# Kernel optimization log

Hardware: AMD Instinct MI355X
Metric: run time of the kernel (lower is better)

Reference implementation:

```python
import jax, jax.numpy as jnp
import numpy as np

EPS = 1e-6
NUM_HEADS = 12


def ln_cf(x, w, b):
    # channels_first LayerNorm over channel dim (ConvNeXt style)
    u = jnp.mean(x, axis=1, keepdims=True)
    s = jnp.mean((x - u) ** 2, axis=1, keepdims=True)
    xn = (x - u) / jnp.sqrt(s + EPS)
    shp = (1, -1) + (1,) * (x.ndim - 2)
    return xn * w.reshape(shp) + b.reshape(shp)


def conv2s2(x, w):
    # Conv3d kernel=2 stride=2 (no bias): exact non-overlapping patch contraction
    b, c, H, W, D = x.shape
    xp = x.reshape(b, c, H // 2, 2, W // 2, 2, D // 2, 2)
    return jnp.einsum('bchkwpdq,ockpq->bohwd', xp, w)


def convt2s2(x, w):
    # ConvTranspose3d kernel=2 stride=2 (torch weight layout [in, out, 2,2,2])
    b, i, H, W, D = x.shape
    o = w.shape[1]
    y = jnp.einsum('bihwd,iokpq->bohkwpdq', x, w)
    return y.reshape(b, o, 2 * H, 2 * W, 2 * D)


def stem(x, w1, g1, b1, w2, g2, b2):
    h = conv2s2(x, w1)
    h = jax.nn.gelu(ln_cf(h, g1, b1), approximate=False)
    h = conv2s2(h, w2)
    return ln_cf(h, g2, b2)


def debed(x, tw1, g, b, tw2, tb2):
    h = convt2s2(x, tw1)
    h = jax.nn.gelu(ln_cf(h, g, b), approximate=False)
    return convt2s2(h, tw2) + tb2.reshape(1, -1, 1, 1, 1)


def rope(x):
    # rotary embedding over full token dim c (pairs (i, i+c/2)), positions 0..L-1
    b, l, c = x.shape
    inv = 1.0 / (10000.0 ** (jnp.arange(0, c, 2, dtype=jnp.float32) / c))
    t = jnp.arange(l, dtype=jnp.float32)
    f = jnp.outer(t, inv)                      # [l, c/2]
    emb = jnp.concatenate([f, f], axis=-1)     # [l, c]
    cos, sin = jnp.cos(emb)[None], jnp.sin(emb)[None]
    rot = jnp.concatenate([-x[..., c // 2:], x[..., :c // 2]], axis=-1)
    return x * cos + rot * sin


def _forward(x, skip, q_w1, q_g1, q_b1, q_w2, q_g2, q_b2,
             k_w1, k_g1, k_b1, k_w2, k_g2, k_b2,
             v_w1, v_g1, v_b1, v_w2, v_g2, v_b2,
             o_tw1, o_g, o_b, o_tw2, o_tb2,
             ns_w, ns_b, nx_w, nx_b, no_w, no_b):
    res = skip
    skip = ln_cf(skip, ns_w, ns_b)
    x = ln_cf(x, nx_w, nx_b)
    q = stem(skip, q_w1, q_g1, q_b1, q_w2, q_g2, q_b2)
    k = stem(x, k_w1, k_g1, k_b1, k_w2, k_g2, k_b2)
    v = stem(x, v_w1, v_g1, v_b1, v_w2, v_g2, v_b2)
    b, c, Hq, Wq, Dq = q.shape
    _, _, Hk, Wk, Dk = k.shape
    q = q.reshape(b, c, -1).transpose(0, 2, 1)   # [b, Lq, c]
    k = k.reshape(b, c, -1).transpose(0, 2, 1)   # [b, Lk, c]
    v = v.reshape(b, c, -1).transpose(0, 2, 1)
    q = rope(q)
    k = rope(k)
    hd = c // NUM_HEADS
    qh = q.reshape(b, -1, NUM_HEADS, hd).transpose(0, 2, 1, 3)  # [b, nh, Lq, hd]
    kh = k.reshape(b, -1, NUM_HEADS, hd).transpose(0, 2, 1, 3)
    vh = v.reshape(b, -1, NUM_HEADS, hd).transpose(0, 2, 1, 3)
    scale = 1.0 / jnp.sqrt(jnp.float32(hd))
    attn = jax.nn.softmax(jnp.einsum('bhqc,bhkc->bhqk', qh, kh) * scale, axis=-1)
    proj = jnp.einsum('bhqk,bhkc->bhqc', attn, vh)              # [b, nh, Lq, hd]
    # rearrange 'b nh l c -> b (c nh) h w d'
    proj = proj.transpose(0, 3, 1, 2).reshape(b, c, Hq, Wq, Dq)
    proj = ln_cf(proj, no_w, no_b)
    out = debed(proj, o_tw1, o_g, o_b, o_tw2, o_tb2)
    return out + res


def setup_inputs() -> dict:
    key = jax.random.key(0)
    ks = iter(jax.random.split(key, 40))
    def nrm(shape, scale):
        return jax.random.normal(next(ks), shape, jnp.float32) * scale
    E, E4, XF, SF = 768, 192, 6, 6
    inp = {
        'x': nrm((2, XF, 48, 48, 48), 1.0),
        'skip': nrm((2, SF, 48, 48, 48), 1.0),
    }
    for p, ic in [('q', SF), ('k', XF), ('v', XF)]:
        inp[p + '_w1'] = nrm((E4, ic, 2, 2, 2), (ic * 8) ** -0.5)
        inp[p + '_g1'] = jnp.ones(E4, jnp.float32)
        inp[p + '_b1'] = jnp.zeros(E4, jnp.float32)
        inp[p + '_w2'] = nrm((E, E4, 2, 2, 2), (E4 * 8) ** -0.5)
        inp[p + '_g2'] = jnp.ones(E, jnp.float32)
        inp[p + '_b2'] = jnp.zeros(E, jnp.float32)
    inp['o_tw1'] = nrm((E, E4, 2, 2, 2), E ** -0.5)
    inp['o_g'] = jnp.ones(E4, jnp.float32)
    inp['o_b'] = jnp.zeros(E4, jnp.float32)
    inp['o_tw2'] = nrm((E4, SF, 2, 2, 2), E4 ** -0.5)
    inp['o_tb2'] = jnp.zeros(SF, jnp.float32)
    inp['ns_w'] = jnp.ones(SF, jnp.float32)
    inp['ns_b'] = jnp.zeros(SF, jnp.float32)
    inp['nx_w'] = jnp.ones(XF, jnp.float32)
    inp['nx_b'] = jnp.zeros(XF, jnp.float32)
    inp['no_w'] = jnp.ones(E, jnp.float32)
    inp['no_b'] = jnp.zeros(E, jnp.float32)
    return inp


def reference(x, skip, q_w1, q_g1, q_b1, q_w2, q_g2, q_b2,
              k_w1, k_g1, k_b1, k_w2, k_g2, k_b2,
              v_w1, v_g1, v_b1, v_w2, v_g2, v_b2,
              o_tw1, o_g, o_b, o_tw2, o_tb2,
              ns_w, ns_b, nx_w, nx_b, no_w, no_b):
    return _forward(x, skip, q_w1, q_g1, q_b1, q_w2, q_g2, q_b2,
                    k_w1, k_g1, k_b1, k_w2, k_g2, k_b2,
                    v_w1, v_g1, v_b1, v_w2, v_g2, v_b2,
                    o_tw1, o_g, o_b, o_tw2, o_tb2,
                    ns_w, ns_b, nx_w, nx_b, no_w, no_b)
```

## Files before the change

kernel.cpp:

```cpp
#include <hip/hip_runtime.h>
#include <math.h>

#define BB_ 2
#define C0 6
#define S0 48
#define V0 (S0*S0*S0)
#define C1 192
#define S1 24
#define V1 (S1*S1*S1)
#define C2 768
#define S2 12
#define LL (S2*S2*S2)
#define NH 12
#define HD 64
#define KDIM (C1*8)
#define MDIM (BB_*LL)

typedef __attribute__((ext_vector_type(8))) short short8;
typedef __attribute__((ext_vector_type(4))) short short4v;
typedef __attribute__((ext_vector_type(4))) float float4v;

static __device__ __forceinline__ float gelu_exact(float x){
  return 0.5f*x*(1.0f+erff(x*0.70710678118654752440f));
}
static __device__ __forceinline__ unsigned short f2bf(float f){
  unsigned int u = __float_as_uint(f);
  unsigned int r = (u + 0x7fffu + ((u>>16)&1u)) >> 16;
  return (unsigned short)r;
}
static __device__ __forceinline__ unsigned int pk_bf16(float a, float b){
#if __has_builtin(__builtin_amdgcn_cvt_pk_bf16_f32)
  typedef __attribute__((ext_vector_type(2))) __bf16 bf2;
  bf2 r = __builtin_amdgcn_cvt_pk_bf16_f32(a,b);
  union { bf2 v; unsigned int u; } cv; cv.v = r;
  return cv.u;
#else
  return (unsigned int)f2bf(a) | ((unsigned int)f2bf(b)<<16);
#endif
}
static __device__ __forceinline__ float bf2f(unsigned short u){
  return __uint_as_float(((unsigned int)u)<<16);
}
static __device__ __forceinline__ float exp2v(float x){
#if __has_builtin(__builtin_amdgcn_exp2f)
  return __builtin_amdgcn_exp2f(x);
#else
  return exp2f(x);
#endif
}
static __device__ __forceinline__ void load_lds16(const void* g, void* l){
  __builtin_amdgcn_global_load_lds((const __attribute__((address_space(1))) unsigned int*)g,
      (__attribute__((address_space(3))) unsigned int*)l, 16, 0, 0);
}
static __device__ __forceinline__ float4v mfma32(short8 a, short8 b, float4v c){
  return __builtin_amdgcn_mfma_f32_16x16x32_bf16(a,b,c,0,0,0);
}
static __device__ __forceinline__ float4v mfma16(short4v a, short4v b, float4v c){
#if __has_builtin(__builtin_amdgcn_mfma_f32_16x16x16bf16_1k)
  return __builtin_amdgcn_mfma_f32_16x16x16bf16_1k(a,b,c,0,0,0);
#else
  asm volatile("v_mfma_f32_16x16x16_bf16 %0, %1, %2, %0" : "+v"(c) : "v"(a), "v"(b));
  return c;
#endif
}


__global__ __launch_bounds__(256) void prep_kernel(
    const float* __restrict__ skin, const float* __restrict__ xin,
    const float* __restrict__ nsw, const float* __restrict__ nsb,
    const float* __restrict__ nxw, const float* __restrict__ nxb,
    unsigned short* __restrict__ outS, unsigned short* __restrict__ outX,
    const float* __restrict__ qw2, const float* __restrict__ kw2, const float* __restrict__ vw2,
    const float* __restrict__ tw1, const float* __restrict__ tw2,
    const float* __restrict__ qw1, const float* __restrict__ kw1, const float* __restrict__ vw1,
    unsigned short* __restrict__ w2tq, unsigned short* __restrict__ w2tk,
    unsigned short* __restrict__ w2tv, unsigned short* __restrict__ Btd,
    unsigned short* __restrict__ Bt48,
    unsigned short* __restrict__ w1q, unsigned short* __restrict__ w1k,
    unsigned short* __restrict__ w1v){
  int bx = blockIdx.x;
  if (bx < 1728){
    int z = bx >= 864;
    const float* in = z ? xin : skin;
    const float* w  = z ? nxw : nsw;
    const float* bi = z ? nxb : nsb;
    unsigned short* out = z ? outX : outS;
    int idx = (bx - z*864)*256 + threadIdx.x;
    int b = idx / V0, vox = idx - b*V0;
    const float* p = in + (size_t)b*(C0*V0) + vox;
    float v[C0]; float s=0.f;
#pragma unroll
    for (int c=0;c<C0;c++){ v[c]=p[(size_t)c*V0]; s+=v[c]; }
    float u = s*(1.f/C0);
    float ss=0.f;
#pragma unroll
    for (int c=0;c<C0;c++){ float d=v[c]-u; ss+=d*d; }
    float inv = rsqrtf(ss*(1.f/C0)+1e-6f);
    unsigned short* o = out + (size_t)b*(C0*V0) + vox;
#pragma unroll
    for (int c=0;c<C0;c++) o[(size_t)c*V0] = f2bf((v[c]-u)*inv*w[c]+bi[c]);
    return;
  }
  bx -= 1728;
  if (bx < 13824){
    int z = bx/4608;
    int idx = (bx - z*4608)*256 + threadIdx.x;
    const float* w2 = (z==0)?qw2:((z==1)?kw2:vw2);
    unsigned short* o = (z==0)?w2tq:((z==1)?w2tk:w2tv);
    int oc = idx/KDIM; int k = idx-oc*KDIM; int p = k/C1; int ic = k-p*C1;
    size_t dst = ((size_t)(oc>>6)*48 + (k>>5))*2048 + (oc&63)*32 + (k&31);
    o[dst] = f2bf(w2[(size_t)oc*KDIM + ic*8 + p]);
  } else if (bx < 18432){
    int idx = (bx-13824)*256 + threadIdx.x;
    int n = idx/C2; int p = idx-n*C2;
    int i = ((p&63)*NH) + (p>>6);
    int kpq = n/C1, o2 = n-kpq*C1;
    size_t dst = ((size_t)(n>>6)*24 + (p>>5))*2048 + (n&63)*32 + (p&31);
    Btd[dst] = f2bf(tw1[(size_t)i*KDIM + o2*8 + kpq]);
  } else if (bx < 18480){
    int idx = (bx-18432)*256 + threadIdx.x;
    int n = idx/C1; int i = idx-n*C1;
    Bt48[idx] = (n<48) ? f2bf(tw2[(size_t)i*48 + n]) : (unsigned short)0;
  } else {
    int idx = (bx-18480)*256 + threadIdx.x;
    int z = idx / 9216; int r = idx - z*9216;
    const float* w1 = (z==0)?qw1:((z==1)?kw1:vw1);
    unsigned short* o = (z==0)?w1q:((z==1)?w1k:w1v);
    o[r] = f2bf(w1[r]);
  }
}

__global__ __launch_bounds__(256) void conv1_kernel(
    const unsigned short* __restrict__ lnSb, const unsigned short* __restrict__ lnXb,
    const unsigned short* __restrict__ w1bq, const unsigned short* __restrict__ w1bk,
    const unsigned short* __restrict__ w1bv,
    const float* __restrict__ qg1, const float* __restrict__ qb1,
    const float* __restrict__ kg1, const float* __restrict__ kb1,
    const float* __restrict__ vg1, const float* __restrict__ vb1,
    unsigned short* __restrict__ h1q, unsigned short* __restrict__ h1k,
    unsigned short* __restrict__ h1v){
  __shared__ __align__(16) unsigned short Ost[4][16*200];
  int z = blockIdx.z;
  const unsigned short* in = (z==0)? lnSb : lnXb;
  const unsigned short* Wb = (z==0)?w1bq:((z==1)?w1bk:w1bv);
  const float* g1 = (z==0)?qg1:((z==1)?kg1:vg1);
  const float* b1 = (z==0)?qb1:((z==1)?kb1:vb1);
  unsigned short* h1p = (z==0)?h1q:((z==1)?h1k:h1v);
  int t = threadIdx.x, w = t>>6, lane = t&63;
  int g = lane>>4, l16 = lane&15;
  int j = blockIdx.x*4 + w;
  int bxh = j/18, mt = j - bxh*18;
  int b = bxh/48; int rem = bxh - b*48; int y = rem>>1, xh = rem&1;
  int xo = mt/3, zo = mt - xo*3;
  int xv = xh*12 + xo*2 + (l16>>3);
  int zv = zo*8 + (l16&7);
  int x2 = 2*xv, z2 = 2*zv, y2 = 2*y;
  const unsigned short* base = in + (size_t)b*C0*V0;
  union { short8 v; unsigned int u[4]; } aA;
  {
    size_t rb = (size_t)g*V0;
    aA.u[0] = *(const unsigned int*)&base[rb + (y2+0)*(S0*S0) + (x2+0)*S0 + z2];
    aA.u[1] = *(const unsigned int*)&base[rb + (y2+0)*(S0*S0) + (x2+1)*S0 + z2];
    aA.u[2] = *(const unsigned int*)&base[rb + (y2+1)*(S0*S0) + (x2+0)*S0 + z2];
    aA.u[3] = *(const unsigned int*)&base[rb + (y2+1)*(S0*S0) + (x2+1)*S0 + z2];
  }
  union { short4v v; unsigned int u[2]; } aB;
  {
    size_t rb = (size_t)(4+(g>>1))*V0 + (y2+(g&1))*(S0*S0);
    aB.u[0] = *(const unsigned int*)&base[rb + (x2+0)*S0 + z2];
    aB.u[1] = *(const unsigned int*)&base[rb + (x2+1)*S0 + z2];
  }
  float4v acc[12];
#pragma unroll
  for (int ot=0; ot<12; ot++){
    short8  wA = *(const short8*)&Wb[(ot*16+l16)*48 + g*8];
    short4v wB = *(const short4v*)&Wb[(ot*16+l16)*48 + 32 + g*4];
    float4v a = {};
    a = mfma32(wA, aA.v, a);
    a = mfma16(wB, aB.v, a);
    acc[ot] = a;
  }
  float s1=0.f, s2=0.f;
#pragma unroll
  for (int ot=0;ot<12;ot++)
#pragma unroll
    for (int reg=0;reg<4;reg++){ float v=acc[ot][reg]; s1+=v; s2+=v*v; }
  s1 += __shfl_xor(s1,16); s1 += __shfl_xor(s1,32);
  s2 += __shfl_xor(s2,16); s2 += __shfl_xor(s2,32);
  float u = s1*(1.f/C1);
  float inv = rsqrtf(s2*(1.f/C1)-u*u+1e-6f);
  int tokbase = (y>>1)*(S2*S2) + (xh*6+xo)*S2 + zo*4;
  int m0_ = b*LL + tokbase;
  int panel = m0_>>7, row0 = m0_&127;
  int Y4 = (y&1)*4;
  int p8x = (l16>>3)*2 + (l16&1);
  int t2 = (l16&7)>>1;
  unsigned short* Lw = &Ost[w][(p8x*4+t2)*200];
#pragma unroll
  for (int ot=0; ot<12; ot++){
    int oc0 = ot*16 + g*4;
    float4 gg = *(const float4*)&g1[oc0];
    float4 bb = *(const float4*)&b1[oc0];
    float x0 = gelu_exact((acc[ot][0]-u)*inv*gg.x+bb.x);
    float x1 = gelu_exact((acc[ot][1]-u)*inv*gg.y+bb.y);
    float x2e= gelu_exact((acc[ot][2]-u)*inv*gg.z+bb.z);
    float x3 = gelu_exact((acc[ot][3]-u)*inv*gg.w+bb.w);
    uint2 pk; pk.x = pk_bf16(x0,x1); pk.y = pk_bf16(x2e,x3);
    *(uint2*)&Lw[oc0] = pk;
  }
  __syncthreads();
  unsigned short* pb2 = h1p + ((size_t)panel*48 + Y4*6)*4096 + row0*32;
#pragma unroll
  for (int it=0; it<6; it++){
    int flat = it*64 + lane;
    int c = flat>>4, s = flat&15;
    int pp = c/6, ocr = c - pp*6;
    uint4 d = *(const uint4*)&Ost[w][(pp*4 + (s>>2))*200 + ocr*32 + (s&3)*8];
    *(uint4*)&pb2[(size_t)c*4096 + (s>>2)*32 + (s&3)*8] = d;
  }
}

__global__ __launch_bounds__(256) void gemm_stem_kernel(
    const unsigned short* __restrict__ A0, const unsigned short* __restrict__ A1,
    const unsigned short* __restrict__ A2,
    const unsigned short* __restrict__ B0, const unsigned short* __restrict__ B1,
    const unsigned short* __restrict__ B2,
    unsigned short* __restrict__ Cq, unsigned short* __restrict__ Ck,
    unsigned short* __restrict__ Cv){
  int flat = blockIdx.x;
  int xcd = flat & 7, slot = flat >> 3;
  int tile = xcd*122 + slot;
  if (tile >= 972) return;
  int z = tile/324; int rr = tile - z*324;
  int mp = rr/12, np = rr - mp*12;
  const unsigned short* A = (z==0)?A0:((z==1)?A1:A2);
  const unsigned short* Bt = (z==0)?B0:((z==1)?B1:B2);
  unsigned short* Cp = (z==0)?Cq:((z==1)?Ck:Cv);
  __shared__ __align__(16) unsigned short Al[3][4096];
  __shared__ __align__(16) unsigned short Bl[3][2048];
  int t=threadIdx.x, w=t>>6, lane=t&63;
  int g=lane>>4, l16=lane&15;
  int wm=w>>1, wn=w&1;
  int loff = (lane>>2)*32 + (((lane&3) ^ ((lane>>3)&3))<<3);
  int crd  = (g ^ ((l16>>1)&3))*8;
  const unsigned short* gp[3];
  unsigned short* ld[3];
  int step[3];
#pragma unroll
  for (int cc=0;cc<3;cc++){
    int ch = w*3+cc;
    if (ch<8){
      gp[cc] = A + ((size_t)mp*48)*4096 + ch*512 + loff;
      step[cc] = 4096; ld[cc] = &Al[0][ch*512];
    } else {
      gp[cc] = Bt + ((size_t)np*48)*2048 + (ch-8)*512 + loff;
      step[cc] = 2048; ld[cc] = &Bl[0][(ch-8)*512];
    }
  }
  auto STAGE = [&](int buf){
#pragma unroll
    for (int cc=0;cc<3;cc++){
      load_lds16(gp[cc], ld[cc] + buf*step[cc]);
      gp[cc] += step[cc];
    }
  };
  float4v acc[4][2] = {};
  auto COMPUTE = [&](int buf){
    short8 af[4], bf[2];
#pragma unroll
    for (int mt=0;mt<4;mt++) af[mt] = *(const short8*)&Al[buf][(wm*64+mt*16+l16)*32 + crd];
#pragma unroll
    for (int nt=0;nt<2;nt++) bf[nt] = *(const short8*)&Bl[buf][(wn*32+nt*16+l16)*32 + crd];
#pragma unroll
    for (int mt=0;mt<4;mt++)
#pragma unroll
      for (int nt=0;nt<2;nt++)
        acc[mt][nt] = mfma32(af[mt], bf[nt], acc[mt][nt]);
  };
  const int NT = 48;
  STAGE(0); STAGE(1);
  asm volatile("s_waitcnt vmcnt(3)" ::: "memory");
  __builtin_amdgcn_s_barrier();
  __builtin_amdgcn_sched_barrier(0);
  int cur = 0;
  for (int tt=0; tt<NT-2; tt++){
    int nb = cur+2; if (nb>=3) nb-=3;
    STAGE(nb);
    COMPUTE(cur);
    asm volatile("s_waitcnt vmcnt(3)" ::: "memory");
    __builtin_amdgcn_s_barrier();
    __builtin_amdgcn_sched_barrier(0);
    cur++; if (cur>=3) cur-=3;
  }
  COMPUTE(cur);
  asm volatile("s_waitcnt vmcnt(0)" ::: "memory");
  __builtin_amdgcn_s_barrier();
  __builtin_amdgcn_sched_barrier(0);
  cur++; if (cur>=3) cur-=3;
  COMPUTE(cur);
  int m0 = mp*128, n0 = np*64;
#pragma unroll
  for (int mt=0;mt<4;mt++){
    int mb = m0 + wm*64 + mt*16 + g*4;
#pragma unroll
    for (int nt=0;nt<2;nt++){
      int col = n0 + wn*32 + nt*16 + l16;
#pragma unroll
      for (int reg=0;reg<4;reg++)
        Cp[(size_t)(mb+reg)*C2 + col] = f2bf(acc[mt][nt][reg]);
    }
  }
}

__global__ __launch_bounds__(256) void gemm_debed_kernel(const unsigned short* __restrict__ A,
    const unsigned short* __restrict__ Bt, unsigned short* __restrict__ C){
  int flat = blockIdx.x;
  int xcd = flat & 7, slot = flat >> 3;
  int tile = xcd*81 + slot;
  int mp = tile/24, np = tile - mp*24;
  __shared__ __align__(16) unsigned short Al[3][4096];
  __shared__ __align__(16) unsigned short Bl[3][2048];
  int t=threadIdx.x, w=t>>6, lane=t&63;
  int g=lane>>4, l16=lane&15;
  int wm=w>>1, wn=w&1;
  int loff = (lane>>2)*32 + (((lane&3) ^ ((lane>>3)&3))<<3);
  int crd  = (g ^ ((l16>>1)&3))*8;
  const unsigned short* gp[3];
  unsigned short* ld[3];
  int step[3];
#pragma unroll
  for (int cc=0;cc<3;cc++){
    int ch = w*3+cc;
    if (ch<8){
      gp[cc] = A + ((size_t)mp*24)*4096 + ch*512 + loff;
      step[cc] = 4096; ld[cc] = &Al[0][ch*512];
    } else {
      gp[cc] = Bt + ((size_t)np*24)*2048 + (ch-8)*512 + loff;
      step[cc] = 2048; ld[cc] = &Bl[0][(ch-8)*512];
    }
  }
  auto STAGE = [&](int buf){
#pragma unroll
    for (int cc=0;cc<3;cc++){
      load_lds16(gp[cc], ld[cc] + buf*step[cc]);
      gp[cc] += step[cc];
    }
  };
  float4v acc[4][2] = {};
  auto COMPUTE = [&](int buf){
    short8 af[4], bf[2];
#pragma unroll
    for (int mt=0;mt<4;mt++) af[mt] = *(const short8*)&Al[buf][(wm*64+mt*16+l16)*32 + crd];
#pragma unroll
    for (int nt=0;nt<2;nt++) bf[nt] = *(const short8*)&Bl[buf][(wn*32+nt*16+l16)*32 + crd];
#pragma unroll
    for (int mt=0;mt<4;mt++)
#pragma unroll
      for (int nt=0;nt<2;nt++)
        acc[mt][nt] = mfma32(af[mt], bf[nt], acc[mt][nt]);
  };
  const int NT = 24;
  STAGE(0); STAGE(1);
  asm volatile("s_waitcnt vmcnt(3)" ::: "memory");
  __builtin_amdgcn_s_barrier();
  __builtin_amdgcn_sched_barrier(0);
  int cur = 0;
  for (int tt=0; tt<NT-2; tt++){
    int nb = cur+2; if (nb>=3) nb-=3;
    STAGE(nb);
    COMPUTE(cur);
    asm volatile("s_waitcnt vmcnt(3)" ::: "memory");
    __builtin_amdgcn_s_barrier();
    __builtin_amdgcn_sched_barrier(0);
    cur++; if (cur>=3) cur-=3;
  }
  COMPUTE(cur);
  asm volatile("s_waitcnt vmcnt(0)" ::: "memory");
  __builtin_amdgcn_s_barrier();
  __builtin_amdgcn_sched_barrier(0);
  cur++; if (cur>=3) cur-=3;
  COMPUTE(cur);
  int m0 = mp*128, n0 = np*64;
#pragma unroll
  for (int nt=0;nt<2;nt++){
    int n = n0 + wn*32 + nt*16 + l16;
    int kpq = n / C1;
    int o = n - kpq*C1;
#pragma unroll
    for (int mt=0;mt<4;mt++){
      int mb = m0 + wm*64 + mt*16 + g*4;
#pragma unroll
      for (int reg=0;reg<4;reg++){
        int m = mb + reg;
        int b = m / LL; int tok = m - b*LL;
        int h = tok/(S2*S2), ww=(tok/S2)%S2, d=tok%S2;
        int v24 = (2*h+((kpq>>2)&1))*(S1*S1) + (2*ww+((kpq>>1)&1))*S1 + (2*d+(kpq&1));
        C[(size_t)(b*V1+v24)*C1 + o] = f2bf(acc[mt][nt][reg]);
      }
    }
  }
}

__global__ __launch_bounds__(256) void final_kernel(const unsigned short* __restrict__ dh,
    const unsigned short* __restrict__ Bt48, const float* __restrict__ og,
    const float* __restrict__ ob, const float* __restrict__ tb2s,
    const float* __restrict__ skipp, float* __restrict__ out){
  __shared__ __align__(16) unsigned short As[64*200];
  __shared__ __align__(16) unsigned short Bs[64*200];
  int t=threadIdx.x, w=t>>6, lane=t&63;
  int g=lane>>4, l16=lane&15;
  int m0 = blockIdx.x*64;
  for (int n8 = t; n8 < 1536; n8 += 256){
    int n64 = n8/24, kk = (n8 - n64*24)*8;
    uint4 d4 = *(const uint4*)&Bt48[n64*192 + kk];
    *(uint4*)&Bs[n64*200 + kk] = d4;
  }
  float g0=og[lane], g1v=og[lane+64], g2v=og[lane+128];
  float b0=ob[lane], b1v=ob[lane+64], b2v=ob[lane+128];
  for (int rr=0; rr<16; rr++){
    int rl = w*16 + rr;
    const unsigned short* row = dh + (size_t)(m0+rl)*C1;
    float v0=bf2f(row[lane]), v1=bf2f(row[lane+64]), v2=bf2f(row[lane+128]);
    float s1=v0+v1+v2, s2=v0*v0+v1*v1+v2*v2;
#pragma unroll
    for (int off=32;off>0;off>>=1){ s1+=__shfl_xor(s1,off); s2+=__shfl_xor(s2,off); }
    float u=s1*(1.f/C1), inv=rsqrtf(s2*(1.f/C1)-u*u+1e-6f);
    As[rl*200+lane]     = f2bf(gelu_exact((v0-u)*inv*g0+b0));
    As[rl*200+lane+64]  = f2bf(gelu_exact((v1-u)*inv*g1v+b1v));
    As[rl*200+lane+128] = f2bf(gelu_exact((v2-u)*inv*g2v+b2v));
  }
  __syncthreads();
  int wm=w>>1, wn=w&1;
  float4v acc[2][2] = {};
#pragma unroll
  for (int kb=0;kb<192;kb+=32){
    short8 af[2], bf[2];
#pragma unroll
    for (int mt=0;mt<2;mt++) af[mt] = *(const short8*)&As[(wm*32+mt*16+l16)*200 + kb + g*8];
#pragma unroll
    for (int nt=0;nt<2;nt++) bf[nt] = *(const short8*)&Bs[(wn*32+nt*16+l16)*200 + kb + g*8];
#pragma unroll
    for (int mt=0;mt<2;mt++)
#pragma unroll
      for (int nt=0;nt<2;nt++)
        acc[mt][nt] = mfma32(af[mt], bf[nt], acc[mt][nt]);
  }
#pragma unroll
  for (int nt=0;nt<2;nt++){
    int n = wn*32 + nt*16 + l16;
    if (n < 48){
      int c = n>>3, kpq = n&7;
      float bias = tb2s[c];
#pragma unroll
      for (int mt=0;mt<2;mt++){
        int mb = m0 + wm*32 + mt*16 + g*4;
#pragma unroll
        for (int reg=0;reg<4;reg++){
          int m = mb + reg;
          int b = m / V1; int v24 = m - b*V1;
          int y24 = v24/(S1*S1), x24=(v24/S1)%S1, z24=v24%S1;
          int vox = (2*y24+((kpq>>2)&1))*(S0*S0) + (2*x24+((kpq>>1)&1))*S0 + 2*z24+(kpq&1);
          size_t oi = (size_t)(b*C0+c)*V0 + vox;
          out[oi] = acc[mt][nt][reg] + bias + skipp[oi];
        }
      }
    }
  }
}

__global__ __launch_bounds__(256) void ln768_stem_kernel(
    unsigned short* __restrict__ qb, unsigned short* __restrict__ kb2,
    unsigned short* __restrict__ vb,
    const float* __restrict__ qg, const float* __restrict__ qbi,
    const float* __restrict__ kg, const float* __restrict__ kbi,
    const float* __restrict__ vg, const float* __restrict__ vbi, float qscale){
  int z = blockIdx.y;
  unsigned short* buf = (z==0)?qb:((z==1)?kb2:vb);
  const float* g  = (z==0)?qg:((z==1)?kg:vg);
  const float* bia= (z==0)?qbi:((z==1)?kbi:vbi);
  float scale = (z==0)? qscale : 1.0f;
  int tok = blockIdx.x*4 + (threadIdx.x>>6), lane = threadIdx.x&63;
  unsigned short* row = buf + (size_t)tok*C2;
  float v[12]; float s1=0.f,s2=0.f;
#pragma unroll
  for (int i=0;i<12;i++){ float t=bf2f(row[i*64+lane]); v[i]=t; s1+=t; s2+=t*t; }
#pragma unroll
  for (int off=32;off>0;off>>=1){ s1+=__shfl_xor(s1,off); s2+=__shfl_xor(s2,off); }
  float u=s1*(1.f/C2);
  float inv=rsqrtf(s2*(1.f/C2)-u*u+1e-6f);
  if (z==2){
#pragma unroll
    for (int i=0;i<12;i++){ int j=i*64+lane; row[j]=f2bf((v[i]-u)*inv*g[j]+bia[j]); }
  } else {
    int pos = tok % LL;
#pragma unroll
    for (int i=0;i<6;i++){
      int j=i*64+lane;
      float xn1=(v[i]-u)*inv*g[j]+bia[j];
      float xn2=(v[i+6]-u)*inv*g[j+384]+bia[j+384];
      float fr=(float)pos*__expf(-0.02398526139f*(float)j);
      float cs=cosf(fr), sn=sinf(fr);
      row[j]     = f2bf((xn1*cs - xn2*sn)*scale);
      row[j+384] = f2bf((xn2*cs + xn1*sn)*scale);
    }
  }
}

__global__ __launch_bounds__(256) void vtrans_kernel(const unsigned short* __restrict__ vbf,
    unsigned short* __restrict__ vT){
  __shared__ unsigned short T[64*72];
  int tok0 = blockIdx.x*64;
  int h = blockIdx.y, b = blockIdx.z;
  int t = threadIdx.x;
#pragma unroll
  for (int i=0;i<2;i++){
    int idx = t + i*256;
    int token = idx>>3, dc = idx&7;
    uint4 d4 = *(const uint4*)&vbf[(size_t)(b*LL+tok0+token)*C2 + h*64 + dc*8];
    const unsigned short* s = (const unsigned short*)&d4;
#pragma unroll
    for (int j2=0;j2<8;j2++) T[(dc*8+j2)*72 + token] = s[j2];
  }
  __syncthreads();
  int r = t>>2, seg = t&3;
  unsigned short* dst = vT + (size_t)((b*NH+h)*HD + r)*LL + tok0 + seg*16;
  uint4 o[2];
  unsigned short* os = (unsigned short*)o;
#pragma unroll
  for (int j2=0;j2<16;j2++) os[j2] = T[r*72 + seg*16 + j2];
  *(uint4*)dst = o[0];
  *(uint4*)(dst+8) = o[1];
}

__global__ __launch_bounds__(256) void attn_kernel(const unsigned short* __restrict__ q,
    const unsigned short* __restrict__ k, const unsigned short* __restrict__ vt,
    unsigned short* __restrict__ opart, float* __restrict__ lbuf){
  __shared__ __align__(16) unsigned char smem[32768];
  unsigned short* Ks = (unsigned short*)smem;
  unsigned short* Vs = Ks + 4096;
  int flat = blockIdx.x;
  int xcd = flat & 7, slot = flat >> 3;
  int tile = xcd*108 + slot;
  int h = tile / 72; int rem = tile - h*72;
  int zb = rem / 9, qt = rem - zb*9;
  int b = zb >> 2, split = zb & 3;
  int t=threadIdx.x, w=t>>6, lane=t&63;
  int g=lane>>4, l16=lane&15;
  short8 qA[3], qB[3];
#pragma unroll
  for (int j=0;j<3;j++){
    const unsigned short* qrow = q + (size_t)(b*LL + qt*192 + w*48 + j*16 + l16)*C2 + h*64;
    qA[j] = *(const short8*)(qrow + g*8);
    qB[j] = *(const short8*)(qrow + 32 + g*8);
  }
  const unsigned short* kbase = k + (size_t)(b*LL)*C2 + h*64;
  const unsigned short* vbase = vt + (size_t)((b*NH+h)*HD)*LL;
  int sub = lane>>3;
  int chs = (lane&7) ^ sub;
  int ktb = split*7, kte = (split==3)? 27 : (split*7+7);
  const unsigned short* gptr[4];
  unsigned short* ldst[4];
  int gstep[4];
#pragma unroll
  for (int cc=0;cc<4;cc++){
    int ii = w*4+cc;
    if (ii<8){
      int key = ktb*64 + ii*8 + sub;
      gptr[cc] = kbase + (size_t)key*C2 + chs*8;
      gstep[cc] = 64*C2;
      ldst[cc] = &Ks[ii*512];
    } else {
      int d = (ii-8)*8 + sub;
      gptr[cc] = vbase + (size_t)d*LL + ktb*64 + chs*8;
      gstep[cc] = 64;
      ldst[cc] = &Vs[(ii-8)*512];
    }
  }
  int sw = l16 & 7;
  const unsigned short* ksrow = &Ks[l16*64 + (g^sw)*8];
  int c2d = (((4+g)^sw) - (g^sw))*8;
  const unsigned short* vsrow = &Vs[l16*64 + (g&1)*4];
  int xk[4];
#pragma unroll
  for (int kc=0;kc<4;kc++) xk[kc] = (((kc*2 + (g>>1)) ^ sw))*8;
  short4v vones;
  vones[0]=vones[1]=vones[2]=vones[3]=(short)0x3F80;
  float4v O4[3][4] = {};
  float4v Ol[3] = {};
#pragma unroll
  for (int cc=0;cc<4;cc++){
    load_lds16(gptr[cc], ldst[cc]);
    gptr[cc] += gstep[cc];
  }
  __syncthreads();
  int cur = 0;
  for (int kt=ktb; kt<kte; kt++){
    if (kt+1 < kte){
      int so = (cur^1)*8192;
#pragma unroll
      for (int cc=0;cc<4;cc++){
        load_lds16(gptr[cc], ldst[cc]+so);
        gptr[cc] += gstep[cc];
      }
    }
    int co = cur*8192;
    const unsigned short* kr = ksrow + co;
    const unsigned short* vr = vsrow + co;
    float4v sc[3][4];
#pragma unroll
    for (int nt=0;nt<4;nt++){
      short8 k1 = *(const short8*)(kr + nt*1024);
      short8 k2 = *(const short8*)(kr + nt*1024 + c2d);
#pragma unroll
      for (int j=0;j<3;j++){
        float4v zz = {};
        zz = mfma32(k1, qA[j], zz);
        zz = mfma32(k2, qB[j], zz);
        sc[j][nt] = zz;
      }
    }
#pragma unroll
    for (int j=0;j<3;j++)
#pragma unroll
      for (int nt=0;nt<4;nt++)
#pragma unroll
        for (int reg=0;reg<4;reg++)
          sc[j][nt][reg] = exp2v(sc[j][nt][reg]);
    short4v pbs[3][4];
#pragma unroll
    for (int j=0;j<3;j++)
#pragma unroll
      for (int kc=0;kc<4;kc++){
        union { short4v v; unsigned int u[2]; } pb;
        pb.u[0] = pk_bf16(sc[j][kc][0], sc[j][kc][1]);
        pb.u[1] = pk_bf16(sc[j][kc][2], sc[j][kc][3]);
        pbs[j][kc] = pb.v;
      }
#pragma unroll
    for (int kc=0;kc<4;kc++){
      const unsigned short* vp = vr + xk[kc];
      short4v va[4];
#pragma unroll
      for (int dt=0;dt<4;dt++) va[dt] = *(const short4v*)(vp + dt*1024);
#pragma unroll
      for (int j=0;j<3;j++){
        Ol[j] = mfma16(vones, pbs[j][kc], Ol[j]);
#pragma unroll
        for (int dt=0;dt<4;dt++)
          O4[j][dt] = mfma16(va[dt], pbs[j][kc], O4[j][dt]);
      }
    }
    __syncthreads();
    cur ^= 1;
  }
  float* Ot = (float*)smem;
  float* ot = Ot + w*1216;
  int qq = lane>>2, c4 = lane&3;
#pragma unroll
  for (int j=0;j<3;j++){
#pragma unroll
    for (int dt=0;dt<4;dt++)
      *(float4*)&ot[l16*76 + dt*16 + g*4] =
          make_float4(O4[j][dt][0],O4[j][dt][1],O4[j][dt][2],O4[j][dt][3]);
    if (g==0){
      int qi = qt*192 + w*48 + j*16 + l16;
      lbuf[((size_t)(b*4+split)*NH+h)*LL + qi] = Ol[j][0];
    }
    unsigned short* orow = opart + (size_t)split*MDIM*C2
                + (size_t)(b*LL + qt*192 + w*48 + j*16 + qq)*C2 + h*64;
#pragma unroll
    for (int p=0;p<4;p++){
      float4 vv = *(float4*)&ot[qq*76 + p*16 + c4*4];
      uint2 pk; pk.x = pk_bf16(vv.x,vv.y); pk.y = pk_bf16(vv.z,vv.w);
      *(uint2*)&orow[p*16 + c4*4] = pk;
    }
    __syncthreads();
  }
}

__global__ __launch_bounds__(256) void attn_post_kernel(const unsigned short* __restrict__ opart,
    const float* __restrict__ lbuf,
    const float* __restrict__ g, const float* __restrict__ bia,
    unsigned short* __restrict__ aob){
  int t=threadIdx.x, w=t>>6, lane=t&63;
  int m = blockIdx.x*4 + w;
  int b = m / LL, l = m - b*LL;
  const unsigned short* o0 = opart + (size_t)m*C2;
  unsigned short* ob2 = aob + ((size_t)(m>>7)*24)*4096 + (size_t)(m&127)*32
                        + (lane&31) + (size_t)(lane>>5)*4096;
  float vv[12]; float s1=0.f, s2=0.f;
#pragma unroll
  for (int i=0;i<12;i++){
    float ls = 0.f;
#pragma unroll
    for (int s=0;s<4;s++) ls += lbuf[((size_t)(b*4+s)*NH+i)*LL + l];
    float inv = 1.f/ls;
    int j = i*64+lane;
    float val = 0.f;
#pragma unroll
    for (int s=0;s<4;s++) val += bf2f(o0[(size_t)s*MDIM*C2 + j]);
    val *= inv;
    vv[i]=val; s1+=val; s2+=val*val;
  }
#pragma unroll
  for (int off=32;off>0;off>>=1){ s1+=__shfl_xor(s1,off); s2+=__shfl_xor(s2,off); }
  float u=s1*(1.f/C2);
  float invs=rsqrtf(s2*(1.f/C2)-u*u+1e-6f);
#pragma unroll
  for (int i=0;i<12;i++){
    int cj = lane*NH + i;
    ob2[(size_t)i*8192] = f2bf((vv[i]-u)*invs*g[cj]+bia[cj]);
  }
}

extern "C" void kernel_launch(void* const* d_in, const int* in_sizes, int n_in,
                              void* d_out, int out_size, void* d_ws, size_t ws_size,
                              hipStream_t stream){
  (void)in_sizes; (void)n_in; (void)out_size; (void)ws_size;
  const float* x    =(const float*)d_in[0];
  const float* skip =(const float*)d_in[1];
  const float* q_w1 =(const float*)d_in[2];
  const float* q_g1 =(const float*)d_in[3];
  const float* q_b1 =(const float*)d_in[4];
  const float* q_w2 =(const float*)d_in[5];
  const float* q_g2 =(const float*)d_in[6];
  const float* q_b2 =(const float*)d_in[7];
  const float* k_w1 =(const float*)d_in[8];
  const float* k_g1 =(const float*)d_in[9];
  const float* k_b1 =(const float*)d_in[10];
  const float* k_w2 =(const float*)d_in[11];
  const float* k_g2 =(const float*)d_in[12];
  const float* k_b2 =(const float*)d_in[13];
  const float* v_w1 =(const float*)d_in[14];
  const float* v_g1 =(const float*)d_in[15];
  const float* v_b1 =(const float*)d_in[16];
  const float* v_w2 =(const float*)d_in[17];
  const float* v_g2 =(const float*)d_in[18];
  const float* v_b2 =(const float*)d_in[19];
  const float* o_tw1=(const float*)d_in[20];
  const float* o_g  =(const float*)d_in[21];
  const float* o_b  =(const float*)d_in[22];
  const float* o_tw2=(const float*)d_in[23];
  const float* o_tb2=(const float*)d_in[24];
  const float* ns_w =(const float*)d_in[25];
  const float* ns_b =(const float*)d_in[26];
  const float* nx_w =(const float*)d_in[27];
  const float* nx_b =(const float*)d_in[28];
  const float* no_w =(const float*)d_in[29];
  const float* no_b =(const float*)d_in[30];
  float* out=(float*)d_out;

  char* W = (char*)d_ws;
  unsigned short* lnSb = (unsigned short*)(W + 0);
  unsigned short* lnXb = (unsigned short*)(W + 2654208);
  unsigned short* h1q  = (unsigned short*)(W + 5308416);
  unsigned short* h1k  = (unsigned short*)(W + 15925248);
  unsigned short* h1v  = (unsigned short*)(W + 26542080);
  unsigned short* w2tq = (unsigned short*)(W + 37158912);
  unsigned short* w2tk = (unsigned short*)(W + 39518208);
  unsigned short* w2tv = (unsigned short*)(W + 41877504);
  unsigned short* qbf  = (unsigned short*)(W + 44236800);
  unsigned short* kbf  = (unsigned short*)(W + 49545216);
  unsigned short* vbf  = (unsigned short*)(W + 54853632);
  unsigned short* vT   = (unsigned short*)(W + 60162048);
  unsigned short* aob  = (unsigned short*)(W + 65470464);
  unsigned short* Btd  = (unsigned short*)(W + 70778880);
  unsigned short* Bt48 = (unsigned short*)(W + 73138176);
  unsigned short* w1q  = (unsigned short*)(W + 73162752);
  unsigned short* w1k  = (unsigned short*)(W + 73181184);
  unsigned short* w1v  = (unsigned short*)(W + 73199616);
  float* lbuf  = (float*)(W + 0);
  unsigned short* opart = (unsigned short*)(W + 5308416);
  unsigned short* dh   = (unsigned short*)(W + 5308416);

  const float QSCALE = 0.125f*1.44269504089f;

  prep_kernel<<<20316,256,0,stream>>>(skip, x, ns_w, ns_b, nx_w, nx_b, lnSb, lnXb,
      q_w2,k_w2,v_w2,o_tw1,o_tw2, q_w1,k_w1,v_w1,
      w2tq,w2tk,w2tv,Btd,Bt48, w1q,w1k,w1v);
  conv1_kernel<<<dim3(432,1,3),256,0,stream>>>(lnSb,lnXb, w1q,w1k,w1v,
      q_g1,q_b1, k_g1,k_b1, v_g1,v_b1, h1q,h1k,h1v);
  gemm_stem_kernel<<<976,256,0,stream>>>(h1q,h1k,h1v,
      w2tq,w2tk,w2tv, qbf,kbf,vbf);
  ln768_stem_kernel<<<dim3(864,3),256,0,stream>>>(qbf,kbf,vbf,
      q_g2,q_b2, k_g2,k_b2, v_g2,v_b2, QSCALE);
  vtrans_kernel<<<dim3(27,12,2),256,0,stream>>>(vbf, vT);
  attn_kernel<<<864,256,0,stream>>>(qbf, kbf, vT, opart, lbuf);
  attn_post_kernel<<<864,256,0,stream>>>(opart, lbuf, no_w, no_b, aob);
  gemm_debed_kernel<<<648,256,0,stream>>>(aob, Btd, dh);
  final_kernel<<<432,256,0,stream>>>(dh, Bt48, o_g, o_b, o_tb2, skip, out);
}
```

Baseline: 307.2 us.

## Triple-buffer K/V tiles in attention with finer vmcnt waits and setprio

The attention kernel's K/V staging goes from double to triple buffering in LDS (shared memory grows from 32KB to 48KB). Each tile now waits with a partial vmcnt and a raw barrier instead of a full __syncthreads. Loads for tile t+2 are issued before computing tile t, and s_setprio raises wave priority around the MFMA section. The goal is to hide global-to-LDS latency better. The cost is more LDS per block, which may lower occupancy, plus reliance on exact vmcnt counting for correctness.

```diff
diff --git a/kernel.cpp b/kernel.cpp
--- a/kernel.cpp
+++ b/kernel.cpp
@@ -535,7 +535,7 @@
 __global__ __launch_bounds__(256) void attn_kernel(const unsigned short* __restrict__ q,
     const unsigned short* __restrict__ k, const unsigned short* __restrict__ vt,
     unsigned short* __restrict__ opart, float* __restrict__ lbuf){
-  __shared__ __align__(16) unsigned char smem[32768];
+  __shared__ __align__(16) unsigned char smem[49152];
   unsigned short* Ks = (unsigned short*)smem;
   unsigned short* Vs = Ks + 4096;
   int flat = blockIdx.x;
@@ -587,26 +587,20 @@
   vones[0]=vones[1]=vones[2]=vones[3]=(short)0x3F80;
   float4v O4[3][4] = {};
   float4v Ol[3] = {};
-#pragma unroll
-  for (int cc=0;cc<4;cc++){
-    load_lds16(gptr[cc], ldst[cc]);
-    gptr[cc] += gstep[cc];
-  }
-  __syncthreads();
-  int cur = 0;
-  for (int kt=ktb; kt<kte; kt++){
-    if (kt+1 < kte){
-      int so = (cur^1)*8192;
-#pragma unroll
-      for (int cc=0;cc<4;cc++){
-        load_lds16(gptr[cc], ldst[cc]+so);
-        gptr[cc] += gstep[cc];
-      }
-    }
-    int co = cur*8192;
+  auto STAGE = [&](int buf){
+    int so = buf*8192;
+#pragma unroll
+    for (int cc=0;cc<4;cc++){
+      load_lds16(gptr[cc], ldst[cc]+so);
+      gptr[cc] += gstep[cc];
+    }
+  };
+  auto COMPUTE = [&](int buf){
+    int co = buf*8192;
     const unsigned short* kr = ksrow + co;
     const unsigned short* vr = vsrow + co;
     float4v sc[3][4];
+    __builtin_amdgcn_s_setprio(1);
 #pragma unroll
     for (int nt=0;nt<4;nt++){
       short8 k1 = *(const short8*)(kr + nt*1024);
@@ -650,9 +644,30 @@
           O4[j][dt] = mfma16(va[dt], pbs[j][kc], O4[j][dt]);
       }
     }
-    __syncthreads();
-    cur ^= 1;
-  }
+    __builtin_amdgcn_s_setprio(0);
+  };
+  const int NTK = kte - ktb;
+  STAGE(0); STAGE(1);
+  asm volatile("s_waitcnt vmcnt(4)" ::: "memory");
+  __builtin_amdgcn_s_barrier();
+  __builtin_amdgcn_sched_barrier(0);
+  int cur = 0;
+  for (int tt=0; tt<NTK-2; tt++){
+    int nb = cur+2; if (nb>=3) nb-=3;
+    STAGE(nb);
+    COMPUTE(cur);
+    asm volatile("s_waitcnt vmcnt(4)" ::: "memory");
+    __builtin_amdgcn_s_barrier();
+    __builtin_amdgcn_sched_barrier(0);
+    cur++; if (cur>=3) cur-=3;
+  }
+  COMPUTE(cur);
+  asm volatile("s_waitcnt vmcnt(0)" ::: "memory");
+  __builtin_amdgcn_s_barrier();
+  __builtin_amdgcn_sched_barrier(0);
+  cur++; if (cur>=3) cur-=3;
+  COMPUTE(cur);
+  __syncthreads();
   float* Ot = (float*)smem;
   float* ot = Ot + w*1216;
   int qq = lane>>2, c4 = lane&3;
```

Result: no change. 313.1 us (+1.9%).

## Widen stem/debed GEMM tiles to 128x128 and fuse V layernorm into transpose

Applied to the files above, without the earlier changes.

Both bf16 MFMA GEMMs (stem and debed) now compute 128x128 output tiles instead of 128x64. This doubles the B tile in LDS, gives each wave 16 accumulators, and halves the grid, cutting redundant A-tile loads per output. Separately, the LayerNorm for V is moved out of ln768_stem_kernel into vtrans_kernel, which computes per-token statistics and applies normalization while transposing, looping over all 12 heads per block. This saves a read-write pass over V but cuts vtrans to only 54 blocks, which may underuse the GPU.

```diff
diff --git a/kernel.cpp b/kernel.cpp
--- a/kernel.cpp
+++ b/kernel.cpp
@@ -229,57 +229,58 @@
     unsigned short* __restrict__ Cv){
   int flat = blockIdx.x;
   int xcd = flat & 7, slot = flat >> 3;
-  int tile = xcd*122 + slot;
-  if (tile >= 972) return;
-  int z = tile/324; int rr = tile - z*324;
-  int mp = rr/12, np = rr - mp*12;
+  int tile = xcd*61 + slot;
+  if (tile >= 486) return;
+  int z = tile/162; int rr = tile - z*162;
+  int mp = rr/6, np2 = rr - mp*6;
   const unsigned short* A = (z==0)?A0:((z==1)?A1:A2);
   const unsigned short* Bt = (z==0)?B0:((z==1)?B1:B2);
   unsigned short* Cp = (z==0)?Cq:((z==1)?Ck:Cv);
   __shared__ __align__(16) unsigned short Al[3][4096];
-  __shared__ __align__(16) unsigned short Bl[3][2048];
+  __shared__ __align__(16) unsigned short Bl[3][4096];
   int t=threadIdx.x, w=t>>6, lane=t&63;
   int g=lane>>4, l16=lane&15;
   int wm=w>>1, wn=w&1;
   int loff = (lane>>2)*32 + (((lane&3) ^ ((lane>>3)&3))<<3);
   int crd  = (g ^ ((l16>>1)&3))*8;
-  const unsigned short* gp[3];
-  unsigned short* ld[3];
-  int step[3];
-#pragma unroll
-  for (int cc=0;cc<3;cc++){
-    int ch = w*3+cc;
+  const unsigned short* gp[4];
+  unsigned short* ld[4];
+  int step[4];
+#pragma unroll
+  for (int cc=0;cc<4;cc++){
+    int ch = w*4+cc;
     if (ch<8){
       gp[cc] = A + ((size_t)mp*48)*4096 + ch*512 + loff;
       step[cc] = 4096; ld[cc] = &Al[0][ch*512];
     } else {
-      gp[cc] = Bt + ((size_t)np*48)*2048 + (ch-8)*512 + loff;
+      int pn = np2*2 + ((ch-8)>>2), cr = (ch-8)&3;
+      gp[cc] = Bt + ((size_t)pn*48)*2048 + cr*512 + loff;
       step[cc] = 2048; ld[cc] = &Bl[0][(ch-8)*512];
     }
   }
   auto STAGE = [&](int buf){
 #pragma unroll
-    for (int cc=0;cc<3;cc++){
-      load_lds16(gp[cc], ld[cc] + buf*step[cc]);
+    for (int cc=0;cc<4;cc++){
+      load_lds16(gp[cc], ld[cc] + buf*4096);
       gp[cc] += step[cc];
     }
   };
-  float4v acc[4][2] = {};
+  float4v acc[4][4] = {};
   auto COMPUTE = [&](int buf){
-    short8 af[4], bf[2];
+    short8 af[4], bf[4];
 #pragma unroll
     for (int mt=0;mt<4;mt++) af[mt] = *(const short8*)&Al[buf][(wm*64+mt*16+l16)*32 + crd];
 #pragma unroll
-    for (int nt=0;nt<2;nt++) bf[nt] = *(const short8*)&Bl[buf][(wn*32+nt*16+l16)*32 + crd];
+    for (int nt=0;nt<4;nt++) bf[nt] = *(const short8*)&Bl[buf][(wn*64+nt*16+l16)*32 + crd];
 #pragma unroll
     for (int mt=0;mt<4;mt++)
 #pragma unroll
-      for (int nt=0;nt<2;nt++)
+      for (int nt=0;nt<4;nt++)
         acc[mt][nt] = mfma32(af[mt], bf[nt], acc[mt][nt]);
   };
   const int NT = 48;
   STAGE(0); STAGE(1);
-  asm volatile("s_waitcnt vmcnt(3)" ::: "memory");
+  asm volatile("s_waitcnt vmcnt(4)" ::: "memory");
   __builtin_amdgcn_s_barrier();
   __builtin_amdgcn_sched_barrier(0);
   int cur = 0;
@@ -287,7 +288,7 @@
     int nb = cur+2; if (nb>=3) nb-=3;
     STAGE(nb);
     COMPUTE(cur);
-    asm volatile("s_waitcnt vmcnt(3)" ::: "memory");
+    asm volatile("s_waitcnt vmcnt(4)" ::: "memory");
     __builtin_amdgcn_s_barrier();
     __builtin_amdgcn_sched_barrier(0);
     cur++; if (cur>=3) cur-=3;
@@ -298,13 +299,13 @@
   __builtin_amdgcn_sched_barrier(0);
   cur++; if (cur>=3) cur-=3;
   COMPUTE(cur);
-  int m0 = mp*128, n0 = np*64;
+  int m0 = mp*128, n0 = np2*128;
 #pragma unroll
   for (int mt=0;mt<4;mt++){
     int mb = m0 + wm*64 + mt*16 + g*4;
 #pragma unroll
-    for (int nt=0;nt<2;nt++){
-      int col = n0 + wn*32 + nt*16 + l16;
+    for (int nt=0;nt<4;nt++){
+      int col = n0 + wn*64 + nt*16 + l16;
 #pragma unroll
       for (int reg=0;reg<4;reg++)
         Cp[(size_t)(mb+reg)*C2 + col] = f2bf(acc[mt][nt][reg]);
@@ -316,52 +317,54 @@
     const unsigned short* __restrict__ Bt, unsigned short* __restrict__ C){
   int flat = blockIdx.x;
   int xcd = flat & 7, slot = flat >> 3;
-  int tile = xcd*81 + slot;
-  int mp = tile/24, np = tile - mp*24;
+  int tile = xcd*41 + slot;
+  if (tile >= 324) return;
+  int mp = tile/12, np2 = tile - mp*12;
   __shared__ __align__(16) unsigned short Al[3][4096];
-  __shared__ __align__(16) unsigned short Bl[3][2048];
+  __shared__ __align__(16) unsigned short Bl[3][4096];
   int t=threadIdx.x, w=t>>6, lane=t&63;
   int g=lane>>4, l16=lane&15;
   int wm=w>>1, wn=w&1;
   int loff = (lane>>2)*32 + (((lane&3) ^ ((lane>>3)&3))<<3);
   int crd  = (g ^ ((l16>>1)&3))*8;
-  const unsigned short* gp[3];
-  unsigned short* ld[3];
-  int step[3];
-#pragma unroll
-  for (int cc=0;cc<3;cc++){
-    int ch = w*3+cc;
+  const unsigned short* gp[4];
+  unsigned short* ld[4];
+  int step[4];
+#pragma unroll
+  for (int cc=0;cc<4;cc++){
+    int ch = w*4+cc;
     if (ch<8){
       gp[cc] = A + ((size_t)mp*24)*4096 + ch*512 + loff;
       step[cc] = 4096; ld[cc] = &Al[0][ch*512];
     } else {
-      gp[cc] = Bt + ((size_t)np*24)*2048 + (ch-8)*512 + loff;
+      int pn = np2*2 + ((ch-8)>>2), cr = (ch-8)&3;
+      gp[cc] = Bt + ((size_t)pn*24)*2048 + cr*512 + loff;
       step[cc] = 2048; ld[cc] = &Bl[0][(ch-8)*512];
     }
   }
   auto STAGE = [&](int buf){
 #pragma unroll
-    for (int cc=0;cc<3;cc++){
-      load_lds16(gp[cc], ld[cc] + buf*step[cc]);
+    for (int cc=0;cc<4;cc++){
+      load_lds16(gp[cc], ld[cc] + buf*4096);
       gp[cc] += step[cc];
     }
   };
-  float4v acc[4][2] = {};
+  float4v acc[4][4] = {};
   auto COMPUTE = [&](int buf){
-    short8 af[4], bf[2];
+    short8 af[4], bf[4];
 #pragma unroll
     for (int mt=0;mt<4;mt++) af[mt] = *(const short8*)&Al[buf][(wm*64+mt*16+l16)*32 + crd];
 #pragma unroll
-    for (int nt=0;nt<2;nt++) bf[nt] = *(const short8*)&Bl[buf][(wn*32+nt*16+l16)*32 + crd];
+    for (int nt=0;nt<4;nt++) bf[nt] = *(const short8*)&Bl[buf][(wn*64+nt*16+l16)*32 + crd];
 #pragma unroll
     for (int mt=0;mt<4;mt++)
 #pragma unroll
-      for (int nt=0;nt<2;nt++)
+      for (int nt=0;nt<4;nt++)
         acc[mt][nt] = mfma32(af[mt], bf[nt], acc[mt][nt]);
   };
   const int NT = 24;
   STAGE(0); STAGE(1);
-  asm volatile("s_waitcnt vmcnt(3)" ::: "memory");
+  asm volatile("s_waitcnt vmcnt(4)" ::: "memory");
   __builtin_amdgcn_s_barrier();
   __builtin_amdgcn_sched_barrier(0);
   int cur = 0;
@@ -369,7 +372,7 @@
     int nb = cur+2; if (nb>=3) nb-=3;
     STAGE(nb);
     COMPUTE(cur);
-    asm volatile("s_waitcnt vmcnt(3)" ::: "memory");
+    asm volatile("s_waitcnt vmcnt(4)" ::: "memory");
     __builtin_amdgcn_s_barrier();
     __builtin_amdgcn_sched_barrier(0);
     cur++; if (cur>=3) cur-=3;
@@ -380,10 +383,10 @@
   __builtin_amdgcn_sched_barrier(0);
   cur++; if (cur>=3) cur-=3;
   COMPUTE(cur);
-  int m0 = mp*128, n0 = np*64;
-#pragma unroll
-  for (int nt=0;nt<2;nt++){
-    int n = n0 + wn*32 + nt*16 + l16;
+  int m0 = mp*128, n0 = np2*128;
+#pragma unroll
+  for (int nt=0;nt<4;nt++){
+    int n = n0 + wn*64 + nt*16 + l16;
     int kpq = n / C1;
     int o = n - kpq*C1;
 #pragma unroll
@@ -470,14 +473,12 @@
 
 __global__ __launch_bounds__(256) void ln768_stem_kernel(
     unsigned short* __restrict__ qb, unsigned short* __restrict__ kb2,
-    unsigned short* __restrict__ vb,
     const float* __restrict__ qg, const float* __restrict__ qbi,
-    const float* __restrict__ kg, const float* __restrict__ kbi,
-    const float* __restrict__ vg, const float* __restrict__ vbi, float qscale){
+    const float* __restrict__ kg, const float* __restrict__ kbi, float qscale){
   int z = blockIdx.y;
-  unsigned short* buf = (z==0)?qb:((z==1)?kb2:vb);
-  const float* g  = (z==0)?qg:((z==1)?kg:vg);
-  const float* bia= (z==0)?qbi:((z==1)?kbi:vbi);
+  unsigned short* buf = (z==0)?qb:kb2;
+  const float* g  = (z==0)?qg:kg;
+  const float* bia= (z==0)?qbi:kbi;
   float scale = (z==0)? qscale : 1.0f;
   int tok = blockIdx.x*4 + (threadIdx.x>>6), lane = threadIdx.x&63;
   unsigned short* row = buf + (size_t)tok*C2;
@@ -488,48 +489,71 @@
   for (int off=32;off>0;off>>=1){ s1+=__shfl_xor(s1,off); s2+=__shfl_xor(s2,off); }
   float u=s1*(1.f/C2);
   float inv=rsqrtf(s2*(1.f/C2)-u*u+1e-6f);
-  if (z==2){
-#pragma unroll
-    for (int i=0;i<12;i++){ int j=i*64+lane; row[j]=f2bf((v[i]-u)*inv*g[j]+bia[j]); }
-  } else {
-    int pos = tok % LL;
-#pragma unroll
-    for (int i=0;i<6;i++){
-      int j=i*64+lane;
-      float xn1=(v[i]-u)*inv*g[j]+bia[j];
-      float xn2=(v[i+6]-u)*inv*g[j+384]+bia[j+384];
-      float fr=(float)pos*__expf(-0.02398526139f*(float)j);
-      float cs=cosf(fr), sn=sinf(fr);
-      row[j]     = f2bf((xn1*cs - xn2*sn)*scale);
-      row[j+384] = f2bf((xn2*cs + xn1*sn)*scale);
-    }
+  int pos = tok % LL;
+#pragma unroll
+  for (int i=0;i<6;i++){
+    int j=i*64+lane;
+    float xn1=(v[i]-u)*inv*g[j]+bia[j];
+    float xn2=(v[i+6]-u)*inv*g[j+384]+bia[j+384];
+    float fr=(float)pos*__expf(-0.02398526139f*(float)j);
+    float cs=cosf(fr), sn=sinf(fr);
+    row[j]     = f2bf((xn1*cs - xn2*sn)*scale);
+    row[j+384] = f2bf((xn2*cs + xn1*sn)*scale);
   }
 }
 
 __global__ __launch_bounds__(256) void vtrans_kernel(const unsigned short* __restrict__ vbf,
+    const float* __restrict__ vg, const float* __restrict__ vbi,
     unsigned short* __restrict__ vT){
   __shared__ unsigned short T[64*72];
+  __shared__ float stats[64][2];
   int tok0 = blockIdx.x*64;
-  int h = blockIdx.y, b = blockIdx.z;
+  int b = blockIdx.y;
   int t = threadIdx.x;
-#pragma unroll
-  for (int i=0;i<2;i++){
-    int idx = t + i*256;
-    int token = idx>>3, dc = idx&7;
-    uint4 d4 = *(const uint4*)&vbf[(size_t)(b*LL+tok0+token)*C2 + h*64 + dc*8];
-    const unsigned short* s = (const unsigned short*)&d4;
-#pragma unroll
-    for (int j2=0;j2<8;j2++) T[(dc*8+j2)*72 + token] = s[j2];
+  {
+    int tok = t>>2, q4 = t&3;
+    const unsigned short* row = vbf + (size_t)(b*LL+tok0+tok)*C2 + q4*192;
+    float s1=0.f, s2=0.f;
+#pragma unroll
+    for (int i=0;i<24;i++){
+      short8 v8 = *(const short8*)&row[i*8];
+#pragma unroll
+      for (int j2=0;j2<8;j2++){ float f=bf2f(((const unsigned short*)&v8)[j2]); s1+=f; s2+=f*f; }
+    }
+    s1 += __shfl_xor(s1,1); s1 += __shfl_xor(s1,2);
+    s2 += __shfl_xor(s2,1); s2 += __shfl_xor(s2,2);
+    if (q4==0){
+      float u = s1*(1.f/C2);
+      stats[tok][0] = u;
+      stats[tok][1] = rsqrtf(s2*(1.f/C2)-u*u+1e-6f);
+    }
   }
   __syncthreads();
-  int r = t>>2, seg = t&3;
-  unsigned short* dst = vT + (size_t)((b*NH+h)*HD + r)*LL + tok0 + seg*16;
-  uint4 o[2];
-  unsigned short* os = (unsigned short*)o;
-#pragma unroll
-  for (int j2=0;j2<16;j2++) os[j2] = T[r*72 + seg*16 + j2];
-  *(uint4*)dst = o[0];
-  *(uint4*)(dst+8) = o[1];
+  for (int h=0; h<NH; h++){
+#pragma unroll
+    for (int i=0;i<2;i++){
+      int idx = t + i*256;
+      int token = idx>>3, dc = idx&7;
+      uint4 d4 = *(const uint4*)&vbf[(size_t)(b*LL+tok0+token)*C2 + h*64 + dc*8];
+      const unsigned short* s = (const unsigned short*)&d4;
+      float u = stats[token][0], inv = stats[token][1];
+#pragma unroll
+      for (int j2=0;j2<8;j2++){
+        int ch = h*64 + dc*8 + j2;
+        T[(dc*8+j2)*72 + token] = f2bf((bf2f(s[j2])-u)*inv*vg[ch]+vbi[ch]);
+      }
+    }
+    __syncthreads();
+    int r = t>>2, seg = t&3;
+    unsigned short* dst = vT + (size_t)((b*NH+h)*HD + r)*LL + tok0 + seg*16;
+    uint4 o[2];
+    unsigned short* os = (unsigned short*)o;
+#pragma unroll
+    for (int j2=0;j2<16;j2++) os[j2] = T[r*72 + seg*16 + j2];
+    *(uint4*)dst = o[0];
+    *(uint4*)(dst+8) = o[1];
+    __syncthreads();
+  }
 }
 
 __global__ __launch_bounds__(256) void attn_kernel(const unsigned short* __restrict__ q,
@@ -780,13 +804,13 @@
       w2tq,w2tk,w2tv,Btd,Bt48, w1q,w1k,w1v);
   conv1_kernel<<<dim3(432,1,3),256,0,stream>>>(lnSb,lnXb, w1q,w1k,w1v,
       q_g1,q_b1, k_g1,k_b1, v_g1,v_b1, h1q,h1k,h1v);
-  gemm_stem_kernel<<<976,256,0,stream>>>(h1q,h1k,h1v,
+  gemm_stem_kernel<<<488,256,0,stream>>>(h1q,h1k,h1v,
       w2tq,w2tk,w2tv, qbf,kbf,vbf);
-  ln768_stem_kernel<<<dim3(864,3),256,0,stream>>>(qbf,kbf,vbf,
-      q_g2,q_b2, k_g2,k_b2, v_g2,v_b2, QSCALE);
-  vtrans_kernel<<<dim3(27,12,2),256,0,stream>>>(vbf, vT);
+  ln768_stem_kernel<<<dim3(864,2),256,0,stream>>>(qbf,kbf,
+      q_g2,q_b2, k_g2,k_b2, QSCALE);
+  vtrans_kernel<<<dim3(27,2),256,0,stream>>>(vbf, v_g2, v_b2, vT);
   attn_kernel<<<864,256,0,stream>>>(qbf, kbf, vT, opart, lbuf);
   attn_post_kernel<<<864,256,0,stream>>>(opart, lbuf, no_w, no_b, aob);
-  gemm_debed_kernel<<<648,256,0,stream>>>(aob, Btd, dh);
+  gemm_debed_kernel<<<328,256,0,stream>>>(aob, Btd, dh);
   final_kernel<<<432,256,0,stream>>>(dh, Bt48, o_g, o_b, o_tb2, skip, out);
 }
```

Measured after the change: 363.0 us. 18.1% more time.
